# Kernel tuning notes

Hardware: AMD Instinct MI355X
Metric: run time of the kernel (lower is better)

The kernel has to match this reference:

```python
import jax, jax.numpy as jnp
import numpy as np

B, C, H, W = 8, 256, 200, 200
N = 256
OUT = 7  # out_size


def setup_inputs() -> dict:
    key = jax.random.key(0)
    kf, kb = jax.random.split(key)
    feature_map = jax.random.normal(kf, (B, C, H, W), dtype=jnp.float32)
    # integer box coords; sort (lo,hi) pairs so x1<=x2, y1<=y2 as the torch
    # slicing semantics require for a non-empty ROI
    raw = jax.random.randint(kb, (B, N, 2, 2), 0, W)
    raw = jnp.sort(raw, axis=-1)
    x1 = raw[..., 0, 0]; x2 = raw[..., 0, 1]
    y1 = raw[..., 1, 0]; y2 = raw[..., 1, 1]
    proposals = jnp.stack([x1, y1, x2, y2], axis=-1).astype(jnp.int32)
    return {"feature_map": feature_map, "proposals": proposals}


def reference(feature_map, proposals):
    # Vectorized equivalent of: per-box clamp -> integer slice -> bilinear
    # F.interpolate(size=(OUT,OUT), align_corners=False).
    Bf, Cf, Hf, Wf = feature_map.shape
    S = OUT
    boxes = proposals.reshape(-1, 4)            # [R,4], R = B*N (loop order: batch, then box)
    R = boxes.shape[0]
    bx1 = jnp.clip(boxes[:, 0], 0, Wf - 1)
    by1 = jnp.clip(boxes[:, 1], 0, Hf - 1)
    bx2 = jnp.clip(boxes[:, 2], 0, Wf - 1)
    by2 = jnp.clip(boxes[:, 3], 0, Hf - 1)
    h = by2 - by1 + 1                            # ROI height (int)
    w = bx2 - bx1 + 1
    # PyTorch bilinear (align_corners=False): src = max((dst+0.5)*scale - 0.5, 0)
    grid = jnp.arange(S, dtype=jnp.float32) + 0.5           # [S]
    src_y = jnp.maximum(grid[None, :] * (h.astype(jnp.float32)[:, None] / S) - 0.5, 0.0)  # [R,S]
    src_x = jnp.maximum(grid[None, :] * (w.astype(jnp.float32)[:, None] / S) - 0.5, 0.0)
    y0f = jnp.floor(src_y); x0f = jnp.floor(src_x)
    wy = src_y - y0f; wx = src_x - x0f                       # bilinear lambdas [R,S]
    y0 = y0f.astype(jnp.int32); x0 = x0f.astype(jnp.int32)
    y1i = jnp.minimum(y0 + 1, (h - 1)[:, None])
    x1i = jnp.minimum(x0 + 1, (w - 1)[:, None])
    # absolute feature-map indices
    ya0 = by1[:, None] + y0;  ya1 = by1[:, None] + y1i       # [R,S]
    xa0 = bx1[:, None] + x0;  xa1 = bx1[:, None] + x1i
    bidx = jnp.arange(R, dtype=jnp.int32) // N               # [R] batch of each ROI
    fm = jnp.transpose(feature_map, (0, 2, 3, 1))            # [B,H,W,C] channels-last gather

    def gather(ya, xa):
        return fm[bidx[:, None, None], ya[:, :, None], xa[:, None, :]]  # [R,S,S,C]

    wy_ = wy[:, :, None, None]
    wx_ = wx[:, None, :, None]
    out = ((1 - wy_) * (1 - wx_) * gather(ya0, xa0)
           + (1 - wy_) * wx_ * gather(ya0, xa1)
           + wy_ * (1 - wx_) * gather(ya1, xa0)
           + wy_ * wx_ * gather(ya1, xa1))                    # [R,S,S,C]
    return jnp.transpose(out, (0, 3, 1, 2))                   # [R,C,S,S]
```

## Files before the change

kernel.cpp:

```cpp
#include <hip/hip_runtime.h>


#define B_DIM 8
#define C_DIM 256
#define H_DIM 200
#define W_DIM 200
#define S_DIM 7
#define NBINS (S_DIM * S_DIM)
#define NROI  256
#define THREADS 512
#define ROWS_HALF0 101
#define ROWS_HALF1 100
#define LDS_BYTES (ROWS_HALF0 * W_DIM * 4)

__global__ __launch_bounds__(THREADS) void roialign_kernel(
    const float* __restrict__ fm,
    const int*   __restrict__ props,
    float*       __restrict__ out)
{
    extern __shared__ float sPlane[];

    const int bid  = blockIdx.x;
    const int half = bid & 1;
    const int c    = (bid >> 1) & (C_DIM - 1);
    const int b    = bid >> 9;

    const int r0      = half ? 100 : 0;
    const int nchunks = (half ? ROWS_HALF1 : ROWS_HALF0) * (W_DIM / 4);

    const int tid = threadIdx.x;

    const float4* __restrict__ src =
        (const float4*)(fm + ((size_t)(b * C_DIM + c)) * (H_DIM * W_DIM) + (size_t)r0 * W_DIM);
    float4* dst = (float4*)sPlane;
    for (int k = tid; k < nchunks; k += THREADS)
        dst[k] = src[k];
    __syncthreads();

    const int4* __restrict__ pbase = (const int4*)props + (size_t)b * NROI;

    for (int item = tid; item < NROI * NBINS; item += THREADS) {
        const int roi = item / NBINS;
        const int bin = item - roi * NBINS;
        const int sy  = bin / S_DIM;
        const int sx  = bin - sy * S_DIM;

        const int4 p = pbase[roi];
        const int bx1 = min(max(p.x, 0), W_DIM - 1);
        const int by1 = min(max(p.y, 0), H_DIM - 1);
        const int bx2 = min(max(p.z, 0), W_DIM - 1);
        const int by2 = min(max(p.w, 0), H_DIM - 1);
        const int h = by2 - by1 + 1;
        const int w = bx2 - bx1 + 1;

        const float src_y = fmaxf(((float)sy + 0.5f) * (float)h * (1.0f / S_DIM) - 0.5f, 0.0f);
        const float y0f = floorf(src_y);
        const float wy  = src_y - y0f;
        const int y0  = (int)y0f;
        const int y1  = min(y0 + 1, h - 1);
        const int ya0 = by1 + y0;
        const int ya1 = by1 + y1;

        const bool mine = half ? (ya0 >= 100) : (ya0 <= 99);
        if (!mine) continue;

        const float src_x = fmaxf(((float)sx + 0.5f) * (float)w * (1.0f / S_DIM) - 0.5f, 0.0f);
        const float x0f = floorf(src_x);
        const float wx  = src_x - x0f;
        const int x0  = (int)x0f;
        const int x1  = min(x0 + 1, w - 1);
        const int xa0 = bx1 + x0;
        const int xa1 = bx1 + x1;

        const int ry0 = ya0 - r0;
        const int ry1 = ya1 - r0;
        const float v00 = sPlane[ry0 * W_DIM + xa0];
        const float v01 = sPlane[ry0 * W_DIM + xa1];
        const float v10 = sPlane[ry1 * W_DIM + xa0];
        const float v11 = sPlane[ry1 * W_DIM + xa1];

        const float w00 = (1.0f - wy) * (1.0f - wx);
        const float w01 = (1.0f - wy) * wx;
        const float w10 = wy * (1.0f - wx);
        const float w11 = wy * wx;

        const int r = b * NROI + roi;
        out[((size_t)r * C_DIM + c) * NBINS + bin] =
            v00 * w00 + v01 * w01 + v10 * w10 + v11 * w11;
    }
}

extern "C" void kernel_launch(void* const* d_in, const int* in_sizes, int n_in,
                              void* d_out, int out_size, void* d_ws, size_t ws_size,
                              hipStream_t stream)
{
    const float* fm    = (const float*)d_in[0];
    const int*   props = (const int*)d_in[1];
    float*       out   = (float*)d_out;

    hipFuncSetAttribute((const void*)roialign_kernel,
                        hipFuncAttributeMaxDynamicSharedMemorySize, LDS_BYTES);

    const int grid = B_DIM * C_DIM * 2;
    roialign_kernel<<<grid, THREADS, LDS_BYTES, stream>>>(fm, props, out);
}
```

Baseline: 557.5 us.

## Precompute per-bin sample records and bucket by row slab for gather kernel

Adds a precompute kernel that computes each ROI bin's packed coordinates, weights and output offset once per batch, and buckets bin indices by 25-row slab using atomic counters. The gather kernel then stages only a 26-row slab of each channel plane into LDS (about 20KB instead of about 80KB) and processes only the bins whose top row falls in that slab. The aim is to stop recomputing coordinates for every channel, stop scanning all bins in every block, and allow higher occupancy. In exchange it adds a memset, an extra kernel launch, workspace traffic for the record table, and a fallback path when the workspace is too small. The order within each bucket depends on atomics, which affects write order but not the results.

```diff
diff --git a/kernel.cpp b/kernel.cpp
--- a/kernel.cpp
+++ b/kernel.cpp
@@ -6,87 +6,185 @@
 #define H_DIM 200
 #define W_DIM 200
 #define S_DIM 7
-#define NBINS (S_DIM * S_DIM)
+#define NBINS 49
 #define NROI  256
-#define THREADS 512
+#define R_TOT (B_DIM * NROI)
+#define IPI   (NROI * NBINS)
+#define NSLAB 8
+#define SLAB_ROWS 25
+#define STAGE_ROWS 26
+#define GTHREADS 256
+
+struct __align__(16) Rec {
+    unsigned int coords;
+    unsigned int obase;
+    float wy, wx;
+};
+
+#define CNT_BYTES   256
+#define TAB_OFF     CNT_BYTES
+#define TAB_BYTES   (B_DIM * IPI * (int)sizeof(Rec))
+#define IDX_OFF     (TAB_OFF + TAB_BYTES)
+#define IDX_BYTES   (B_DIM * NSLAB * IPI * 2)
+#define WS_NEED     ((size_t)(IDX_OFF + IDX_BYTES))
+
+__global__ __launch_bounds__(256) void precompute_kernel(
+    const int4* __restrict__ props,
+    Rec* __restrict__ tab,
+    unsigned short* __restrict__ idxl,
+    int* __restrict__ cnt)
+{
+    const int gid = blockIdx.x * 256 + threadIdx.x;
+    if (gid >= R_TOT * NBINS) return;
+    const int roi = gid / NBINS;
+    const int bin = gid - roi * NBINS;
+    const int b   = roi >> 8;
+    const int sy  = bin / S_DIM;
+    const int sx  = bin - sy * S_DIM;
+
+    const int4 p = props[roi];
+    const int bx1 = min(max(p.x, 0), W_DIM - 1);
+    const int by1 = min(max(p.y, 0), H_DIM - 1);
+    const int bx2 = min(max(p.z, 0), W_DIM - 1);
+    const int by2 = min(max(p.w, 0), H_DIM - 1);
+    const int h = by2 - by1 + 1;
+    const int w = bx2 - bx1 + 1;
+
+    const float qy = (float)h / (float)S_DIM;
+    const float qx = (float)w / (float)S_DIM;
+    const float src_y = fmaxf(((float)sy + 0.5f) * qy - 0.5f, 0.0f);
+    const float src_x = fmaxf(((float)sx + 0.5f) * qx - 0.5f, 0.0f);
+    const float y0f = floorf(src_y);
+    const float x0f = floorf(src_x);
+    const int y0 = (int)y0f;
+    const int x0 = (int)x0f;
+    const int y1 = min(y0 + 1, h - 1);
+    const int x1 = min(x0 + 1, w - 1);
+    const int ya0 = by1 + y0, ya1 = by1 + y1;
+    const int xa0 = bx1 + x0, xa1 = bx1 + x1;
+
+    Rec rec;
+    rec.coords = (unsigned)ya0 | ((unsigned)xa0 << 8) |
+                 ((unsigned)ya1 << 16) | ((unsigned)xa1 << 24);
+    rec.obase  = (unsigned)((roi & (NROI - 1)) * (C_DIM * NBINS) + bin);
+    rec.wy = src_y - y0f;
+    rec.wx = src_x - x0f;
+
+    const int item = gid - b * IPI;
+    tab[gid] = rec;
+
+    const int slab = ya0 / SLAB_ROWS;
+    const int pos  = atomicAdd(&cnt[b * NSLAB + slab], 1);
+    idxl[(b * NSLAB + slab) * IPI + pos] = (unsigned short)item;
+}
+
+__global__ __launch_bounds__(GTHREADS) void roialign_gather(
+    const float* __restrict__ fm,
+    const Rec*   __restrict__ tab,
+    const unsigned short* __restrict__ idxl,
+    const int*   __restrict__ cnt,
+    float*       __restrict__ out)
+{
+    __shared__ float sPlane[STAGE_ROWS * W_DIM];
+
+    const int bid  = blockIdx.x;
+    const int slab = bid & 7;
+    const int c    = (bid >> 3) & (C_DIM - 1);
+    const int b    = bid >> 11;
+    const int r0   = slab * SLAB_ROWS;
+    const int nrows = (slab == NSLAB - 1) ? SLAB_ROWS : STAGE_ROWS;
+    const int nch   = nrows * (W_DIM / 4);
+
+    const float4* __restrict__ src =
+        (const float4*)(fm + ((size_t)(b * C_DIM + c)) * (H_DIM * W_DIM) + (size_t)r0 * W_DIM);
+    float4* dst4 = (float4*)sPlane;
+    for (int k = threadIdx.x; k < nch; k += GTHREADS)
+        dst4[k] = src[k];
+
+    const int n = cnt[b * NSLAB + slab];
+    __syncthreads();
+
+    const unsigned short* __restrict__ il = idxl + (b * NSLAB + slab) * IPI;
+    const Rec* __restrict__ tb = tab + b * IPI;
+    float* __restrict__ outb =
+        out + (size_t)b * ((size_t)NROI * C_DIM * NBINS) + (size_t)c * NBINS;
+
+    for (int t = threadIdx.x; t < n; t += GTHREADS) {
+        const int item = il[t];
+        const uint4 rv = *(const uint4*)(tb + item);
+        const int ya0 = rv.x & 255;
+        const int xa0 = (rv.x >> 8) & 255;
+        const int ya1 = (rv.x >> 16) & 255;
+        const int xa1 = rv.x >> 24;
+        const float wy = __uint_as_float(rv.z);
+        const float wx = __uint_as_float(rv.w);
+        const int ry0 = ya0 - r0;
+        const int ry1 = ya1 - r0;
+
+        const float v00 = sPlane[ry0 * W_DIM + xa0];
+        const float v01 = sPlane[ry0 * W_DIM + xa1];
+        const float v10 = sPlane[ry1 * W_DIM + xa0];
+        const float v11 = sPlane[ry1 * W_DIM + xa1];
+
+        const float top = v00 + (v01 - v00) * wx;
+        const float bot = v10 + (v11 - v10) * wx;
+        outb[rv.y] = top + (bot - top) * wy;
+    }
+}
+
 #define ROWS_HALF0 101
-#define ROWS_HALF1 100
-#define LDS_BYTES (ROWS_HALF0 * W_DIM * 4)
-
-__global__ __launch_bounds__(THREADS) void roialign_kernel(
-    const float* __restrict__ fm,
-    const int*   __restrict__ props,
-    float*       __restrict__ out)
-{
-    extern __shared__ float sPlane[];
-
+#define FB_LDS (ROWS_HALF0 * W_DIM * 4)
+#define FB_THREADS 512
+
+__global__ __launch_bounds__(FB_THREADS) void roialign_fallback(
+    const float* __restrict__ fm, const int* __restrict__ props, float* __restrict__ out)
+{
+    extern __shared__ float sP[];
     const int bid  = blockIdx.x;
     const int half = bid & 1;
     const int c    = (bid >> 1) & (C_DIM - 1);
     const int b    = bid >> 9;
-
-    const int r0      = half ? 100 : 0;
-    const int nchunks = (half ? ROWS_HALF1 : ROWS_HALF0) * (W_DIM / 4);
-
-    const int tid = threadIdx.x;
+    const int r0   = half ? 100 : 0;
+    const int nch  = (half ? (H_DIM - 100) : ROWS_HALF0) * (W_DIM / 4);
 
     const float4* __restrict__ src =
         (const float4*)(fm + ((size_t)(b * C_DIM + c)) * (H_DIM * W_DIM) + (size_t)r0 * W_DIM);
-    float4* dst = (float4*)sPlane;
-    for (int k = tid; k < nchunks; k += THREADS)
-        dst[k] = src[k];
+    float4* dst4 = (float4*)sP;
+    for (int k = threadIdx.x; k < nch; k += FB_THREADS) dst4[k] = src[k];
     __syncthreads();
 
     const int4* __restrict__ pbase = (const int4*)props + (size_t)b * NROI;
-
-    for (int item = tid; item < NROI * NBINS; item += THREADS) {
+    for (int item = threadIdx.x; item < NROI * NBINS; item += FB_THREADS) {
         const int roi = item / NBINS;
         const int bin = item - roi * NBINS;
-        const int sy  = bin / S_DIM;
-        const int sx  = bin - sy * S_DIM;
-
+        const int sy = bin / S_DIM, sx = bin - sy * S_DIM;
         const int4 p = pbase[roi];
         const int bx1 = min(max(p.x, 0), W_DIM - 1);
         const int by1 = min(max(p.y, 0), H_DIM - 1);
         const int bx2 = min(max(p.z, 0), W_DIM - 1);
         const int by2 = min(max(p.w, 0), H_DIM - 1);
-        const int h = by2 - by1 + 1;
-        const int w = bx2 - bx1 + 1;
-
-        const float src_y = fmaxf(((float)sy + 0.5f) * (float)h * (1.0f / S_DIM) - 0.5f, 0.0f);
+        const int h = by2 - by1 + 1, w = bx2 - bx1 + 1;
+        const float src_y = fmaxf(((float)sy + 0.5f) * ((float)h / (float)S_DIM) - 0.5f, 0.0f);
         const float y0f = floorf(src_y);
-        const float wy  = src_y - y0f;
-        const int y0  = (int)y0f;
-        const int y1  = min(y0 + 1, h - 1);
-        const int ya0 = by1 + y0;
-        const int ya1 = by1 + y1;
-
+        const float wy = src_y - y0f;
+        const int y0 = (int)y0f;
+        const int y1 = min(y0 + 1, h - 1);
+        const int ya0 = by1 + y0, ya1 = by1 + y1;
         const bool mine = half ? (ya0 >= 100) : (ya0 <= 99);
         if (!mine) continue;
-
-        const float src_x = fmaxf(((float)sx + 0.5f) * (float)w * (1.0f / S_DIM) - 0.5f, 0.0f);
+        const float src_x = fmaxf(((float)sx + 0.5f) * ((float)w / (float)S_DIM) - 0.5f, 0.0f);
         const float x0f = floorf(src_x);
-        const float wx  = src_x - x0f;
-        const int x0  = (int)x0f;
-        const int x1  = min(x0 + 1, w - 1);
-        const int xa0 = bx1 + x0;
-        const int xa1 = bx1 + x1;
-
-        const int ry0 = ya0 - r0;
-        const int ry1 = ya1 - r0;
-        const float v00 = sPlane[ry0 * W_DIM + xa0];
-        const float v01 = sPlane[ry0 * W_DIM + xa1];
-        const float v10 = sPlane[ry1 * W_DIM + xa0];
-        const float v11 = sPlane[ry1 * W_DIM + xa1];
-
-        const float w00 = (1.0f - wy) * (1.0f - wx);
-        const float w01 = (1.0f - wy) * wx;
-        const float w10 = wy * (1.0f - wx);
-        const float w11 = wy * wx;
-
-        const int r = b * NROI + roi;
-        out[((size_t)r * C_DIM + c) * NBINS + bin] =
-            v00 * w00 + v01 * w01 + v10 * w10 + v11 * w11;
+        const float wx = src_x - x0f;
+        const int x0 = (int)x0f;
+        const int x1 = min(x0 + 1, w - 1);
+        const int xa0 = bx1 + x0, xa1 = bx1 + x1;
+        const float v00 = sP[(ya0 - r0) * W_DIM + xa0];
+        const float v01 = sP[(ya0 - r0) * W_DIM + xa1];
+        const float v10 = sP[(ya1 - r0) * W_DIM + xa0];
+        const float v11 = sP[(ya1 - r0) * W_DIM + xa1];
+        const float top = v00 + (v01 - v00) * wx;
+        const float bot = v10 + (v11 - v10) * wx;
+        out[(((size_t)(b * NROI + roi)) * C_DIM + c) * NBINS + bin] = top + (bot - top) * wy;
     }
 }
 
@@ -98,9 +196,19 @@
     const int*   props = (const int*)d_in[1];
     float*       out   = (float*)d_out;
 
-    hipFuncSetAttribute((const void*)roialign_kernel,
-                        hipFuncAttributeMaxDynamicSharedMemorySize, LDS_BYTES);
-
-    const int grid = B_DIM * C_DIM * 2;
-    roialign_kernel<<<grid, THREADS, LDS_BYTES, stream>>>(fm, props, out);
-}
+    if (ws_size >= WS_NEED) {
+        int* cnt = (int*)d_ws;
+        Rec* tab = (Rec*)((char*)d_ws + TAB_OFF);
+        unsigned short* idxl = (unsigned short*)((char*)d_ws + IDX_OFF);
+
+        hipMemsetAsync(cnt, 0, CNT_BYTES, stream);
+        precompute_kernel<<<(R_TOT * NBINS) / 256, 256, 0, stream>>>(
+            (const int4*)props, tab, idxl, cnt);
+        roialign_gather<<<B_DIM * C_DIM * NSLAB, GTHREADS, 0, stream>>>(
+            fm, tab, idxl, cnt, out);
+    } else {
+        hipFuncSetAttribute((const void*)roialign_fallback,
+                            hipFuncAttributeMaxDynamicSharedMemorySize, FB_LDS);
+        roialign_fallback<<<B_DIM * C_DIM * 2, FB_THREADS, FB_LDS, stream>>>(fm, props, out);
+    }
+}
```

After: 1.063 ms. 90.7% more time.
